# Performance work log

Measured on AMD Instinct MI355X. Metric: run time of the kernel, lower is better.

The kernel has to match this reference:

```python
import jax, jax.numpy as jnp
import numpy as np

STAGE_NUM = 5
BETA = 1.0
EPS = 1e-6


def _em_refine(cls, proto):
    # cls: [b, d]; proto: [k, d]. Matches torch einsum('bd,bkd->bk') with
    # batch-replicated prototypes == cls @ proto.T (no (b,k,d) materialization).
    p = proto
    for _ in range(STAGE_NUM):
        r = jax.nn.softmax(cls @ p.T, axis=1)          # [b, k]
        p = r.T @ cls                                   # [k, d]
        p = p / (jnp.linalg.norm(p, axis=1, keepdims=True) + EPS)
    return p


def setup_inputs() -> dict:
    key = jax.random.key(0)
    k1, k2 = jax.random.split(key)
    b, d, k = 8192, 1024, 512
    cls = jax.random.normal(k1, (b, d), dtype=jnp.float32)
    proto = jax.random.normal(k2, (k, d), dtype=jnp.float32)
    # __init__ normalizes prototypes to unit norm (with 1e-6 in denominator)
    proto = proto / (1e-6 + jnp.linalg.norm(proto, axis=1, keepdims=True))
    return {"cls": cls, "prototypes": proto}


def reference(cls, prototypes):
    # EM loop runs under torch.no_grad() -> stop_gradient here.
    new_proto = jax.lax.stop_gradient(_em_refine(cls, prototypes))  # [k, d]
    dot = cls @ new_proto.T                                          # [b, k]
    r = jax.nn.softmax(dot, axis=1)
    z_recon = r @ new_proto                                          # [b, d]
    z_out = BETA * z_recon + cls
    return (r, z_out)
```

## Files before the change

### kernel.cpp

```cpp
#include <hip/hip_runtime.h>

typedef short v8s __attribute__((ext_vector_type(8)));
typedef _Float16 v8h __attribute__((ext_vector_type(8)));
typedef float v4f __attribute__((ext_vector_type(4)));

typedef __attribute__((address_space(1))) const void* as1_void_cp;
typedef __attribute__((address_space(3))) void* as3_void_p;

__device__ __forceinline__ unsigned short f2bf(float x) {
  union { float f; unsigned int u; } v; v.f = x;
  unsigned int r = v.u + 0x7fffu + ((v.u >> 16) & 1u);
  return (unsigned short)(r >> 16);
}
__device__ __forceinline__ float bf2f(unsigned short h) {
  union { unsigned int u; float f; } v; v.u = ((unsigned int)h) << 16;
  return v.f;
}
__device__ __forceinline__ unsigned short f2h(float x) {
  _Float16 h = (_Float16)x;
  return __builtin_bit_cast(unsigned short, h);
}

template <bool ADD, bool F16>
__global__ __launch_bounds__(256) void gemm_bt(
    const unsigned short* __restrict__ A, const unsigned short* __restrict__ B,
    float* __restrict__ C, const float* __restrict__ Cadd,
    int N, int lda, int ldb, int klen, size_t csplit) {
  __shared__ __align__(16) unsigned short As[128 * 64];
  __shared__ __align__(16) unsigned short Bs[128 * 64];
  const int tid = threadIdx.x;
  const int bn = blockIdx.x * 128, bm = blockIdx.y * 128;
  const int k0 = blockIdx.z * klen;
  float* Cp = C + (size_t)blockIdx.z * csplit;

  const unsigned short* ag0 = A + (size_t)(bm + (tid >> 2)) * lda + ((tid & 3) << 3) + k0;
  const unsigned short* ag1 = ag0 + (size_t)64 * lda;
  const unsigned short* bg0 = B + (size_t)(bn + (tid >> 2)) * ldb + ((tid & 3) << 3) + k0;
  const unsigned short* bg1 = bg0 + (size_t)64 * ldb;
  unsigned short* al0 = As + tid * 8;
  unsigned short* al1 = As + 2048 + tid * 8;
  unsigned short* al2 = As + 4096 + tid * 8;
  unsigned short* al3 = As + 6144 + tid * 8;
  unsigned short* bl0 = Bs + tid * 8;
  unsigned short* bl1 = Bs + 2048 + tid * 8;
  unsigned short* bl2 = Bs + 4096 + tid * 8;
  unsigned short* bl3 = Bs + 6144 + tid * 8;

  const int lane = tid & 63;
  const int q = lane >> 4, m15 = lane & 15;
  const int w = tid >> 6;
  const int wr = (w >> 1) * 64, wc = (w & 1) * 64;

  v4f acc[4][4];
#pragma unroll
  for (int i = 0; i < 4; ++i)
#pragma unroll
    for (int j = 0; j < 4; ++j) acc[i][j] = 0.f;

  for (int kk = 0; kk < klen; kk += 64) {
    __builtin_amdgcn_global_load_lds((as1_void_cp)(ag0 + kk), (as3_void_p)al0, 16, 0, 0);
    __builtin_amdgcn_global_load_lds((as1_void_cp)(ag1 + kk), (as3_void_p)al1, 16, 0, 0);
    __builtin_amdgcn_global_load_lds((as1_void_cp)(ag0 + kk + 32), (as3_void_p)al2, 16, 0, 0);
    __builtin_amdgcn_global_load_lds((as1_void_cp)(ag1 + kk + 32), (as3_void_p)al3, 16, 0, 0);
    __builtin_amdgcn_global_load_lds((as1_void_cp)(bg0 + kk), (as3_void_p)bl0, 16, 0, 0);
    __builtin_amdgcn_global_load_lds((as1_void_cp)(bg1 + kk), (as3_void_p)bl1, 16, 0, 0);
    __builtin_amdgcn_global_load_lds((as1_void_cp)(bg0 + kk + 32), (as3_void_p)bl2, 16, 0, 0);
    __builtin_amdgcn_global_load_lds((as1_void_cp)(bg1 + kk + 32), (as3_void_p)bl3, 16, 0, 0);
    __syncthreads();
#pragma unroll
    for (int h = 0; h < 2; ++h) {
      v8s af[4], bf[4];
#pragma unroll
      for (int i = 0; i < 4; ++i)
        af[i] = *(const v8s*)(As + h * 4096 + (wr + i * 16 + m15) * 32 + q * 8);
#pragma unroll
      for (int j = 0; j < 4; ++j)
        bf[j] = *(const v8s*)(Bs + h * 4096 + (wc + j * 16 + m15) * 32 + q * 8);
#pragma unroll
      for (int i = 0; i < 4; ++i)
#pragma unroll
        for (int j = 0; j < 4; ++j) {
          if constexpr (F16)
            acc[i][j] = __builtin_amdgcn_mfma_f32_16x16x32_f16(
                __builtin_bit_cast(v8h, af[i]), __builtin_bit_cast(v8h, bf[j]), acc[i][j], 0, 0, 0);
          else
            acc[i][j] = __builtin_amdgcn_mfma_f32_16x16x32_bf16(af[i], bf[j], acc[i][j], 0, 0, 0);
        }
    }
    __syncthreads();
  }

#pragma unroll
  for (int i = 0; i < 4; ++i) {
#pragma unroll
    for (int j = 0; j < 4; ++j) {
      const int col = bn + wc + j * 16 + m15;
#pragma unroll
      for (int rr = 0; rr < 4; ++rr) {
        const int row = bm + wr + i * 16 + q * 4 + rr;
        const size_t idx = (size_t)row * N + col;
        float v = acc[i][j][rr];
        if (ADD) v += Cadd[idx];
        Cp[idx] = v;
      }
    }
  }
}

__global__ __launch_bounds__(256) void gemm_bt3(
    const unsigned short* __restrict__ Ah, const unsigned short* __restrict__ Al,
    const unsigned short* __restrict__ Bh, const unsigned short* __restrict__ Bl,
    float* __restrict__ C, int N, int lda, int ldb, int klen, size_t csplit) {
  __shared__ __align__(16) unsigned short Ash[128 * 32];
  __shared__ __align__(16) unsigned short Asl[128 * 32];
  __shared__ __align__(16) unsigned short Bsh[128 * 32];
  __shared__ __align__(16) unsigned short Bsl[128 * 32];
  const int tid = threadIdx.x;
  const int bn = blockIdx.x * 128, bm = blockIdx.y * 128;
  const int k0 = blockIdx.z * klen;
  float* Cp = C + (size_t)blockIdx.z * csplit;

  const size_t aoff = (size_t)(bm + (tid >> 2)) * lda + ((tid & 3) << 3) + k0;
  const size_t boff = (size_t)(bn + (tid >> 2)) * ldb + ((tid & 3) << 3) + k0;
  const unsigned short* agh0 = Ah + aoff;
  const unsigned short* agh1 = agh0 + (size_t)64 * lda;
  const unsigned short* agl0 = Al + aoff;
  const unsigned short* agl1 = agl0 + (size_t)64 * lda;
  const unsigned short* bgh0 = Bh + boff;
  const unsigned short* bgh1 = bgh0 + (size_t)64 * ldb;
  const unsigned short* bgl0 = Bl + boff;
  const unsigned short* bgl1 = bgl0 + (size_t)64 * ldb;

  const int lane = tid & 63;
  const int q = lane >> 4, m15 = lane & 15;
  const int w = tid >> 6;
  const int wr = (w >> 1) * 64, wc = (w & 1) * 64;

  v4f acc[4][4];
#pragma unroll
  for (int i = 0; i < 4; ++i)
#pragma unroll
    for (int j = 0; j < 4; ++j) acc[i][j] = 0.f;

  for (int kk = 0; kk < klen; kk += 32) {
    __builtin_amdgcn_global_load_lds((as1_void_cp)(agh0 + kk), (as3_void_p)(Ash + tid * 8), 16, 0, 0);
    __builtin_amdgcn_global_load_lds((as1_void_cp)(agh1 + kk), (as3_void_p)(Ash + 2048 + tid * 8), 16, 0, 0);
    __builtin_amdgcn_global_load_lds((as1_void_cp)(agl0 + kk), (as3_void_p)(Asl + tid * 8), 16, 0, 0);
    __builtin_amdgcn_global_load_lds((as1_void_cp)(agl1 + kk), (as3_void_p)(Asl + 2048 + tid * 8), 16, 0, 0);
    __builtin_amdgcn_global_load_lds((as1_void_cp)(bgh0 + kk), (as3_void_p)(Bsh + tid * 8), 16, 0, 0);
    __builtin_amdgcn_global_load_lds((as1_void_cp)(bgh1 + kk), (as3_void_p)(Bsh + 2048 + tid * 8), 16, 0, 0);
    __builtin_amdgcn_global_load_lds((as1_void_cp)(bgl0 + kk), (as3_void_p)(Bsl + tid * 8), 16, 0, 0);
    __builtin_amdgcn_global_load_lds((as1_void_cp)(bgl1 + kk), (as3_void_p)(Bsl + 2048 + tid * 8), 16, 0, 0);
    __syncthreads();
    v8s afh[4], afl[4], bfh[4], bfl[4];
#pragma unroll
    for (int i = 0; i < 4; ++i) {
      const int ro = (wr + i * 16 + m15) * 32 + q * 8;
      afh[i] = *(const v8s*)(Ash + ro);
      afl[i] = *(const v8s*)(Asl + ro);
    }
#pragma unroll
    for (int j = 0; j < 4; ++j) {
      const int ro = (wc + j * 16 + m15) * 32 + q * 8;
      bfh[j] = *(const v8s*)(Bsh + ro);
      bfl[j] = *(const v8s*)(Bsl + ro);
    }
#pragma unroll
    for (int i = 0; i < 4; ++i)
#pragma unroll
      for (int j = 0; j < 4; ++j) {
        acc[i][j] = __builtin_amdgcn_mfma_f32_16x16x32_bf16(afh[i], bfh[j], acc[i][j], 0, 0, 0);
        acc[i][j] = __builtin_amdgcn_mfma_f32_16x16x32_bf16(afh[i], bfl[j], acc[i][j], 0, 0, 0);
        acc[i][j] = __builtin_amdgcn_mfma_f32_16x16x32_bf16(afl[i], bfh[j], acc[i][j], 0, 0, 0);
      }
    __syncthreads();
  }

#pragma unroll
  for (int i = 0; i < 4; ++i) {
#pragma unroll
    for (int j = 0; j < 4; ++j) {
      const int col = bn + wc + j * 16 + m15;
#pragma unroll
      for (int rr = 0; rr < 4; ++rr) {
        const int row = bm + wr + i * 16 + q * 4 + rr;
        Cp[(size_t)row * N + col] = acc[i][j][rr];
      }
    }
  }
}

__global__ __launch_bounds__(256) void cast_split_transpose_cls(
    const float* __restrict__ cls,
    unsigned short* __restrict__ ch, unsigned short* __restrict__ cl,
    unsigned short* __restrict__ cTh, unsigned short* __restrict__ cTl) {
  __shared__ unsigned short th[64][72];
  __shared__ unsigned short tl[64][72];
  const int d0 = blockIdx.x * 64, b0 = blockIdx.y * 64;
  const int t = threadIdx.x;
#pragma unroll
  for (int i = 0; i < 4; ++i) {
    int flat = t + i * 256;
    int bl_ = flat >> 4;
    int dl = (flat & 15) << 2;
    float4 v = *(const float4*)(cls + (size_t)(b0 + bl_) * 1024 + d0 + dl);
    ushort4 h, l;
    h.x = f2bf(v.x); l.x = f2bf(v.x - bf2f(h.x));
    h.y = f2bf(v.y); l.y = f2bf(v.y - bf2f(h.y));
    h.z = f2bf(v.z); l.z = f2bf(v.z - bf2f(h.z));
    h.w = f2bf(v.w); l.w = f2bf(v.w - bf2f(h.w));
    *(ushort4*)(ch + (size_t)(b0 + bl_) * 1024 + d0 + dl) = h;
    *(ushort4*)(cl + (size_t)(b0 + bl_) * 1024 + d0 + dl) = l;
    th[bl_][dl] = h.x; th[bl_][dl + 1] = h.y; th[bl_][dl + 2] = h.z; th[bl_][dl + 3] = h.w;
    tl[bl_][dl] = l.x; tl[bl_][dl + 1] = l.y; tl[bl_][dl + 2] = l.z; tl[bl_][dl + 3] = l.w;
  }
  __syncthreads();
#pragma unroll
  for (int i = 0; i < 4; ++i) {
    int flat = t + i * 256;
    int dl = flat >> 4;
    int bl_ = (flat & 15) << 2;
    ushort4 h = make_ushort4(th[bl_][dl], th[bl_ + 1][dl], th[bl_ + 2][dl], th[bl_ + 3][dl]);
    ushort4 l = make_ushort4(tl[bl_][dl], tl[bl_ + 1][dl], tl[bl_ + 2][dl], tl[bl_ + 3][dl]);
    *(ushort4*)(cTh + (size_t)(d0 + dl) * 8192 + b0 + bl_) = h;
    *(ushort4*)(cTl + (size_t)(d0 + dl) * 8192 + b0 + bl_) = l;
  }
}

__global__ __launch_bounds__(256) void split_f32(const float* __restrict__ in,
                                                 unsigned short* __restrict__ hi,
                                                 unsigned short* __restrict__ lo) {
  const size_t i = (size_t)(blockIdx.x * blockDim.x + threadIdx.x) * 4;
  float4 v = *(const float4*)(in + i);
  ushort4 h, l;
  h.x = f2bf(v.x); l.x = f2bf(v.x - bf2f(h.x));
  h.y = f2bf(v.y); l.y = f2bf(v.y - bf2f(h.y));
  h.z = f2bf(v.z); l.z = f2bf(v.z - bf2f(h.z));
  h.w = f2bf(v.w); l.w = f2bf(v.w - bf2f(h.w));
  *(ushort4*)(hi + i) = h;
  *(ushort4*)(lo + i) = l;
}

__global__ __launch_bounds__(256) void fuse_to_f16_dual(
    const unsigned short* __restrict__ h0, const unsigned short* __restrict__ l0,
    unsigned short* __restrict__ o0,
    const unsigned short* __restrict__ h1, const unsigned short* __restrict__ l1,
    unsigned short* __restrict__ o1) {
  const int half = blockIdx.x >> 12;
  const unsigned short* hi = half ? h1 : h0;
  const unsigned short* lo = half ? l1 : l0;
  unsigned short* out = half ? o1 : o0;
  const size_t i = ((size_t)(blockIdx.x & 4095) * 256 + threadIdx.x) * 8;
  ushort4 ha = *(const ushort4*)(hi + i);
  ushort4 hb = *(const ushort4*)(hi + i + 4);
  ushort4 la = *(const ushort4*)(lo + i);
  ushort4 lb = *(const ushort4*)(lo + i + 4);
  ushort4 oa, ob;
  oa.x = f2h(bf2f(ha.x) + bf2f(la.x)); oa.y = f2h(bf2f(ha.y) + bf2f(la.y));
  oa.z = f2h(bf2f(ha.z) + bf2f(la.z)); oa.w = f2h(bf2f(ha.w) + bf2f(la.w));
  ob.x = f2h(bf2f(hb.x) + bf2f(lb.x)); ob.y = f2h(bf2f(hb.y) + bf2f(lb.y));
  ob.z = f2h(bf2f(hb.z) + bf2f(lb.z)); ob.w = f2h(bf2f(hb.w) + bf2f(lb.w));
  *(ushort4*)(out + i) = oa;
  *(ushort4*)(out + i + 4) = ob;
}

__device__ __forceinline__ void online_merge(float& m, float& s, float m2, float s2) {
  float nm = fmaxf(m, m2);
  s = s * __expf(m - nm) + s2 * __expf(m2 - nm);
  m = nm;
}

__global__ __launch_bounds__(256) void colsoftmax_stats(
    const float* __restrict__ SP0, const float* __restrict__ SP1,
    float4* __restrict__ MS) {
  __shared__ float4 red[4][64];
  const int lane = threadIdx.x & 63, w = threadIdx.x >> 6;
  const int b = blockIdx.x * 128 + lane * 2;
  const int c0 = blockIdx.y * 64 + w * 16;
  const float2* x0 = (const float2*)(SP0 + (size_t)c0 * 8192 + b);
  const float2* x1 = (const float2*)(SP1 + (size_t)c0 * 8192 + b);
  float m0 = -3.4e38f, m1 = -3.4e38f, s0 = 0.f, s1 = 0.f;
#pragma unroll
  for (int i = 0; i < 16; ++i) {
    float2 a = x0[(size_t)i * 4096];
    float2 bb = x1[(size_t)i * 4096];
    float v0 = a.x + bb.x, v1 = a.y + bb.y;
    float nm0 = fmaxf(m0, v0);
    s0 = s0 * __expf(m0 - nm0) + __expf(v0 - nm0); m0 = nm0;
    float nm1 = fmaxf(m1, v1);
    s1 = s1 * __expf(m1 - nm1) + __expf(v1 - nm1); m1 = nm1;
  }
  red[w][lane] = make_float4(m0, s0, m1, s1);
  __syncthreads();
  if (w == 0) {
#pragma unroll
    for (int k = 1; k < 4; ++k) {
      float4 r = red[k][lane];
      online_merge(m0, s0, r.x, r.y);
      online_merge(m1, s1, r.z, r.w);
    }
    MS[(size_t)blockIdx.y * 4096 + (b >> 1)] = make_float4(m0, s0, m1, s1);
  }
}

template <bool F16>
__global__ __launch_bounds__(256) void colsoftmax_write(
    const float* __restrict__ SP0, const float* __restrict__ SP1,
    const float4* __restrict__ MS,
    unsigned short* __restrict__ rh, unsigned short* __restrict__ rl) {
  const int lane = threadIdx.x & 63, w = threadIdx.x >> 6;
  const int b = blockIdx.x * 128 + lane * 2;
  const int c0 = blockIdx.y * 64 + w * 16;
  float m0 = -3.4e38f, m1 = -3.4e38f, s0 = 0.f, s1 = 0.f;
#pragma unroll
  for (int k = 0; k < 8; ++k) {
    float4 r = MS[(size_t)k * 4096 + (b >> 1)];
    online_merge(m0, s0, r.x, r.y);
    online_merge(m1, s1, r.z, r.w);
  }
  const float inv0 = 1.f / s0, inv1 = 1.f / s1;
  const float2* x0 = (const float2*)(SP0 + (size_t)c0 * 8192 + b);
  const float2* x1 = (const float2*)(SP1 + (size_t)c0 * 8192 + b);
#pragma unroll
  for (int i = 0; i < 16; ++i) {
    float2 a = x0[(size_t)i * 4096];
    float2 bb = x1[(size_t)i * 4096];
    float r0 = __expf(a.x + bb.x - m0) * inv0;
    float r1 = __expf(a.y + bb.y - m1) * inv1;
    const size_t idx = (size_t)(c0 + i) * 8192 + b;
    if constexpr (F16) {
      *(ushort2*)(rh + idx) = make_ushort2(f2h(r0), f2h(r1));
    } else {
      unsigned short h0 = f2bf(r0), h1 = f2bf(r1);
      *(ushort2*)(rh + idx) = make_ushort2(h0, h1);
      *(ushort2*)(rl + idx) = make_ushort2(f2bf(r0 - bf2f(h0)), f2bf(r1 - bf2f(h1)));
    }
  }
}

__global__ __launch_bounds__(256) void softmax_rows(const float* __restrict__ SP0,
                                                    const float* __restrict__ SP1,
                                                    float* __restrict__ r_out,
                                                    unsigned short* __restrict__ r_g) {
  const int w = threadIdx.x >> 6, lane = threadIdx.x & 63;
  const int row = blockIdx.x * 4 + w;
  const size_t off = (size_t)row * 512 + lane * 8;
  float4 v0 = *(const float4*)(SP0 + off);
  float4 v1 = *(const float4*)(SP0 + off + 4);
  float4 u0 = *(const float4*)(SP1 + off);
  float4 u1 = *(const float4*)(SP1 + off + 4);
  v0.x += u0.x; v0.y += u0.y; v0.z += u0.z; v0.w += u0.w;
  v1.x += u1.x; v1.y += u1.y; v1.z += u1.z; v1.w += u1.w;
  float m = fmaxf(fmaxf(fmaxf(v0.x, v0.y), fmaxf(v0.z, v0.w)),
                  fmaxf(fmaxf(v1.x, v1.y), fmaxf(v1.z, v1.w)));
  for (int off2 = 32; off2; off2 >>= 1) m = fmaxf(m, __shfl_xor(m, off2));
  float e0 = __expf(v0.x - m), e1 = __expf(v0.y - m), e2 = __expf(v0.z - m), e3 = __expf(v0.w - m);
  float e4 = __expf(v1.x - m), e5 = __expf(v1.y - m), e6 = __expf(v1.z - m), e7 = __expf(v1.w - m);
  float s = e0 + e1 + e2 + e3 + e4 + e5 + e6 + e7;
  for (int off2 = 32; off2; off2 >>= 1) s += __shfl_xor(s, off2);
  const float inv = 1.f / s;
  e0 *= inv; e1 *= inv; e2 *= inv; e3 *= inv; e4 *= inv; e5 *= inv; e6 *= inv; e7 *= inv;
  float* rp = r_out + off;
  *(float4*)rp = make_float4(e0, e1, e2, e3);
  *(float4*)(rp + 4) = make_float4(e4, e5, e6, e7);
  unsigned short* bp = r_g + off;
  *(ushort4*)bp = make_ushort4(f2h(e0), f2h(e1), f2h(e2), f2h(e3));
  *(ushort4*)(bp + 4) = make_ushort4(f2h(e4), f2h(e5), f2h(e6), f2h(e7));
}

__global__ __launch_bounds__(256) void reduce_normalize(const float* __restrict__ Pp,
                                                        unsigned short* __restrict__ pg,
                                                        unsigned short* __restrict__ pTg) {
  __shared__ float red[4];
  const int c = blockIdx.x, t = threadIdx.x;
  float ax = 0.f, ay = 0.f, az = 0.f, aw = 0.f;
#pragma unroll
  for (int s = 0; s < 16; ++s) {
    const float4 v = *(const float4*)(Pp + ((size_t)s * 512 + c) * 1024 + t * 4);
    ax += v.x; ay += v.y; az += v.z; aw += v.w;
  }
  float ss = ax * ax + ay * ay + az * az + aw * aw;
  for (int off = 32; off; off >>= 1) ss += __shfl_xor(ss, off);
  const int w = t >> 6, lane = t & 63;
  if (!lane) red[w] = ss;
  __syncthreads();
  const float tot = red[0] + red[1] + red[2] + red[3];
  const float scale = 1.f / (sqrtf(tot) + 1e-6f);
  ax *= scale; ay *= scale; az *= scale; aw *= scale;
  *(ushort4*)(pg + (size_t)c * 1024 + t * 4) =
      make_ushort4(f2h(ax), f2h(ay), f2h(az), f2h(aw));
  pTg[(size_t)(t * 4 + 0) * 512 + c] = f2h(ax);
  pTg[(size_t)(t * 4 + 1) * 512 + c] = f2h(ay);
  pTg[(size_t)(t * 4 + 2) * 512 + c] = f2h(az);
  pTg[(size_t)(t * 4 + 3) * 512 + c] = f2h(aw);
}

extern "C" void kernel_launch(void* const* d_in, const int* in_sizes, int n_in,
                              void* d_out, int out_size, void* d_ws, size_t ws_size,
                              hipStream_t stream) {
  const float* cls = (const float*)d_in[0];
  const float* proto = (const float*)d_in[1];
  float* out_r = (float*)d_out;
  float* out_z = out_r + (size_t)8192 * 512;

  char* w = (char*)d_ws;
  unsigned short* cls_h = (unsigned short*)w; w += (size_t)8192 * 1024 * 2;
  unsigned short* cls_l = (unsigned short*)w; w += (size_t)8192 * 1024 * 2;
  unsigned short* clsT_h = (unsigned short*)w; w += (size_t)1024 * 8192 * 2;
  unsigned short* clsT_l = (unsigned short*)w; w += (size_t)1024 * 8192 * 2;
  unsigned short* p_h = (unsigned short*)w; w += (size_t)512 * 1024 * 2;
  unsigned short* p_l = (unsigned short*)w; w += (size_t)512 * 1024 * 2;
  unsigned short* p_g = (unsigned short*)w; w += (size_t)512 * 1024 * 2;
  unsigned short* pT_g = (unsigned short*)w; w += (size_t)1024 * 512 * 2;
  unsigned short* rT_h = (unsigned short*)w; w += (size_t)512 * 8192 * 2;
  unsigned short* rT_l = (unsigned short*)w; w += (size_t)512 * 8192 * 2;
  float4* MS = (float4*)w; w += (size_t)8 * 4096 * 16;
  float* SP = (float*)w;
  float* SP1 = SP + (size_t)512 * 8192;
  unsigned short* cls_g = cls_l;
  unsigned short* clsT_g = clsT_l;

  cast_split_transpose_cls<<<dim3(16, 128), 256, 0, stream>>>(cls, cls_h, cls_l, clsT_h, clsT_l);
  split_f32<<<512, 256, 0, stream>>>(proto, p_h, p_l);

  gemm_bt3<<<dim3(64, 4, 2), 256, 0, stream>>>(p_h, p_l, cls_h, cls_l, SP,
                                               8192, 1024, 1024, 512,
                                               (size_t)512 * 8192);
  colsoftmax_stats<<<dim3(64, 8), 256, 0, stream>>>(SP, SP1, MS);
  colsoftmax_write<false><<<dim3(64, 8), 256, 0, stream>>>(SP, SP1, MS, rT_h, rT_l);
  gemm_bt3<<<dim3(8, 4, 16), 256, 0, stream>>>(rT_h, rT_l, clsT_h, clsT_l, SP,
                                               1024, 8192, 8192, 512,
                                               (size_t)512 * 1024);
  fuse_to_f16_dual<<<8192, 256, 0, stream>>>(cls_h, cls_l, cls_g, clsT_h, clsT_l, clsT_g);
  reduce_normalize<<<512, 256, 0, stream>>>(SP, p_g, pT_g);

  for (int it = 0; it < 4; ++it) {
    gemm_bt<false, true><<<dim3(64, 4, 2), 256, 0, stream>>>(p_g, cls_g, SP, nullptr,
                                                             8192, 1024, 1024, 512,
                                                             (size_t)512 * 8192);
    colsoftmax_stats<<<dim3(64, 8), 256, 0, stream>>>(SP, SP1, MS);
    colsoftmax_write<true><<<dim3(64, 8), 256, 0, stream>>>(SP, SP1, MS, rT_h, nullptr);
    gemm_bt<false, true><<<dim3(8, 4, 16), 256, 0, stream>>>(rT_h, clsT_g, SP, nullptr,
                                                             1024, 8192, 8192, 512,
                                                             (size_t)512 * 1024);
    reduce_normalize<<<512, 256, 0, stream>>>(SP, p_g, pT_g);
  }

  gemm_bt<false, true><<<dim3(4, 64, 2), 256, 0, stream>>>(cls_g, p_g, SP, nullptr,
                                                           512, 1024, 1024, 512,
                                                           (size_t)8192 * 512);
  softmax_rows<<<2048, 256, 0, stream>>>(SP, SP + (size_t)8192 * 512, out_r, rT_h);
  gemm_bt<true, true><<<dim3(8, 64, 1), 256, 0, stream>>>(rT_h, pT_g, out_z, cls,
                                                          1024, 512, 512, 512, 0);
}
```

Measured before the change: 494.6 us.

## Compute EM logits row-major and fuse row softmax with LDS transpose

The EM-step logits GEMM now produces a [b,k] row-major score matrix (operands swapped), so the softmax over k becomes a row softmax done in one kernel with wave shuffles. The result is transposed through shared memory and written as rT, replacing the two-pass column-softmax stats/write kernels and the MS scratch buffer. This removes one launch and one full re-read of the split-K partial scores per iteration. It costs a 33KB-66KB LDS tile per block, and the logits GEMM runs with a different output shape and grid. reduce_normalize_hl is added but never called.

After: 487.0 us. Within noise of the previous version (-1.5%).

```diff
diff --git a/kernel.cpp b/kernel.cpp
--- a/kernel.cpp
+++ b/kernel.cpp
@@ -264,77 +264,64 @@
   *(ushort4*)(out + i + 4) = ob;
 }
 
-__device__ __forceinline__ void online_merge(float& m, float& s, float m2, float s2) {
-  float nm = fmaxf(m, m2);
-  s = s * __expf(m - nm) + s2 * __expf(m2 - nm);
-  m = nm;
-}
-
-__global__ __launch_bounds__(256) void colsoftmax_stats(
+template <bool HILO>
+__global__ __launch_bounds__(512) void rowsoftmax_T(
     const float* __restrict__ SP0, const float* __restrict__ SP1,
-    float4* __restrict__ MS) {
-  __shared__ float4 red[4][64];
-  const int lane = threadIdx.x & 63, w = threadIdx.x >> 6;
-  const int b = blockIdx.x * 128 + lane * 2;
-  const int c0 = blockIdx.y * 64 + w * 16;
-  const float2* x0 = (const float2*)(SP0 + (size_t)c0 * 8192 + b);
-  const float2* x1 = (const float2*)(SP1 + (size_t)c0 * 8192 + b);
-  float m0 = -3.4e38f, m1 = -3.4e38f, s0 = 0.f, s1 = 0.f;
-#pragma unroll
-  for (int i = 0; i < 16; ++i) {
-    float2 a = x0[(size_t)i * 4096];
-    float2 bb = x1[(size_t)i * 4096];
-    float v0 = a.x + bb.x, v1 = a.y + bb.y;
-    float nm0 = fmaxf(m0, v0);
-    s0 = s0 * __expf(m0 - nm0) + __expf(v0 - nm0); m0 = nm0;
-    float nm1 = fmaxf(m1, v1);
-    s1 = s1 * __expf(m1 - nm1) + __expf(v1 - nm1); m1 = nm1;
-  }
-  red[w][lane] = make_float4(m0, s0, m1, s1);
+    unsigned short* __restrict__ rTh, unsigned short* __restrict__ rTl) {
+  __shared__ __align__(16) unsigned short th[32 * 520];
+  __shared__ __align__(16) unsigned short tl[HILO ? 32 * 520 : 8];
+  const int t = threadIdx.x;
+  const int lane = t & 63, w = t >> 6;
+  const int b0 = blockIdx.x * 32;
+#pragma unroll
+  for (int k = 0; k < 4; ++k) {
+    const int bl = w * 4 + k;
+    const int row = b0 + bl;
+    const size_t off = (size_t)row * 512 + lane * 8;
+    float4 v0 = *(const float4*)(SP0 + off);
+    float4 v1 = *(const float4*)(SP0 + off + 4);
+    float4 u0 = *(const float4*)(SP1 + off);
+    float4 u1 = *(const float4*)(SP1 + off + 4);
+    float e[8];
+    e[0] = v0.x + u0.x; e[1] = v0.y + u0.y; e[2] = v0.z + u0.z; e[3] = v0.w + u0.w;
+    e[4] = v1.x + u1.x; e[5] = v1.y + u1.y; e[6] = v1.z + u1.z; e[7] = v1.w + u1.w;
+    float m = fmaxf(fmaxf(fmaxf(e[0], e[1]), fmaxf(e[2], e[3])),
+                    fmaxf(fmaxf(e[4], e[5]), fmaxf(e[6], e[7])));
+    for (int o = 32; o; o >>= 1) m = fmaxf(m, __shfl_xor(m, o));
+    float s = 0.f;
+#pragma unroll
+    for (int i = 0; i < 8; ++i) { e[i] = __expf(e[i] - m); s += e[i]; }
+    for (int o = 32; o; o >>= 1) s += __shfl_xor(s, o);
+    const float inv = 1.f / s;
+    unsigned short ph[8], pl[8];
+#pragma unroll
+    for (int i = 0; i < 8; ++i) {
+      const float r = e[i] * inv;
+      if constexpr (HILO) {
+        ph[i] = f2bf(r);
+        pl[i] = f2bf(r - bf2f(ph[i]));
+      } else {
+        ph[i] = f2h(r);
+      }
+    }
+    *(v8s*)&th[bl * 520 + lane * 8] = *(v8s*)ph;
+    if constexpr (HILO) *(v8s*)&tl[bl * 520 + lane * 8] = *(v8s*)pl;
+  }
   __syncthreads();
-  if (w == 0) {
-#pragma unroll
-    for (int k = 1; k < 4; ++k) {
-      float4 r = red[k][lane];
-      online_merge(m0, s0, r.x, r.y);
-      online_merge(m1, s1, r.z, r.w);
-    }
-    MS[(size_t)blockIdx.y * 4096 + (b >> 1)] = make_float4(m0, s0, m1, s1);
-  }
-}
-
-template <bool F16>
-__global__ __launch_bounds__(256) void colsoftmax_write(
-    const float* __restrict__ SP0, const float* __restrict__ SP1,
-    const float4* __restrict__ MS,
-    unsigned short* __restrict__ rh, unsigned short* __restrict__ rl) {
-  const int lane = threadIdx.x & 63, w = threadIdx.x >> 6;
-  const int b = blockIdx.x * 128 + lane * 2;
-  const int c0 = blockIdx.y * 64 + w * 16;
-  float m0 = -3.4e38f, m1 = -3.4e38f, s0 = 0.f, s1 = 0.f;
-#pragma unroll
-  for (int k = 0; k < 8; ++k) {
-    float4 r = MS[(size_t)k * 4096 + (b >> 1)];
-    online_merge(m0, s0, r.x, r.y);
-    online_merge(m1, s1, r.z, r.w);
-  }
-  const float inv0 = 1.f / s0, inv1 = 1.f / s1;
-  const float2* x0 = (const float2*)(SP0 + (size_t)c0 * 8192 + b);
-  const float2* x1 = (const float2*)(SP1 + (size_t)c0 * 8192 + b);
-#pragma unroll
-  for (int i = 0; i < 16; ++i) {
-    float2 a = x0[(size_t)i * 4096];
-    float2 bb = x1[(size_t)i * 4096];
-    float r0 = __expf(a.x + bb.x - m0) * inv0;
-    float r1 = __expf(a.y + bb.y - m1) * inv1;
-    const size_t idx = (size_t)(c0 + i) * 8192 + b;
-    if constexpr (F16) {
-      *(ushort2*)(rh + idx) = make_ushort2(f2h(r0), f2h(r1));
-    } else {
-      unsigned short h0 = f2bf(r0), h1 = f2bf(r1);
-      *(ushort2*)(rh + idx) = make_ushort2(h0, h1);
-      *(ushort2*)(rl + idx) = make_ushort2(f2bf(r0 - bf2f(h0)), f2bf(r1 - bf2f(h1)));
-    }
+  const int c = t;
+  unsigned short uh[32];
+#pragma unroll
+  for (int b = 0; b < 32; ++b) uh[b] = th[b * 520 + c];
+#pragma unroll
+  for (int q = 0; q < 4; ++q)
+    *(v8s*)(rTh + (size_t)c * 8192 + b0 + q * 8) = *(v8s*)&uh[q * 8];
+  if constexpr (HILO) {
+    unsigned short ul[32];
+#pragma unroll
+    for (int b = 0; b < 32; ++b) ul[b] = tl[b * 520 + c];
+#pragma unroll
+    for (int q = 0; q < 4; ++q)
+      *(v8s*)(rTl + (size_t)c * 8192 + b0 + q * 8) = *(v8s*)&ul[q * 8];
   }
 }
 
@@ -395,6 +382,34 @@
   pTg[(size_t)(t * 4 + 3) * 512 + c] = f2h(aw);
 }
 
+__global__ __launch_bounds__(256) void reduce_normalize_hl(const float* __restrict__ Pp,
+                                                           unsigned short* __restrict__ ph,
+                                                           unsigned short* __restrict__ pl) {
+  __shared__ float red[4];
+  const int c = blockIdx.x, t = threadIdx.x;
+  float ax = 0.f, ay = 0.f, az = 0.f, aw = 0.f;
+#pragma unroll
+  for (int s = 0; s < 16; ++s) {
+    const float4 v = *(const float4*)(Pp + ((size_t)s * 512 + c) * 1024 + t * 4);
+    ax += v.x; ay += v.y; az += v.z; aw += v.w;
+  }
+  float ss = ax * ax + ay * ay + az * az + aw * aw;
+  for (int off = 32; off; off >>= 1) ss += __shfl_xor(ss, off);
+  const int w = t >> 6, lane = t & 63;
+  if (!lane) red[w] = ss;
+  __syncthreads();
+  const float tot = red[0] + red[1] + red[2] + red[3];
+  const float scale = 1.f / (sqrtf(tot) + 1e-6f);
+  ax *= scale; ay *= scale; az *= scale; aw *= scale;
+  ushort4 h, l;
+  h.x = f2bf(ax); l.x = f2bf(ax - bf2f(h.x));
+  h.y = f2bf(ay); l.y = f2bf(ay - bf2f(h.y));
+  h.z = f2bf(az); l.z = f2bf(az - bf2f(h.z));
+  h.w = f2bf(aw); l.w = f2bf(aw - bf2f(h.w));
+  *(ushort4*)(ph + (size_t)c * 1024 + t * 4) = h;
+  *(ushort4*)(pl + (size_t)c * 1024 + t * 4) = l;
+}
+
 extern "C" void kernel_launch(void* const* d_in, const int* in_sizes, int n_in,
                               void* d_out, int out_size, void* d_ws, size_t ws_size,
                               hipStream_t stream) {
@@ -414,20 +429,18 @@
   unsigned short* pT_g = (unsigned short*)w; w += (size_t)1024 * 512 * 2;
   unsigned short* rT_h = (unsigned short*)w; w += (size_t)512 * 8192 * 2;
   unsigned short* rT_l = (unsigned short*)w; w += (size_t)512 * 8192 * 2;
-  float4* MS = (float4*)w; w += (size_t)8 * 4096 * 16;
   float* SP = (float*)w;
-  float* SP1 = SP + (size_t)512 * 8192;
+  float* SP1 = SP + (size_t)8192 * 512;
   unsigned short* cls_g = cls_l;
   unsigned short* clsT_g = clsT_l;
 
   cast_split_transpose_cls<<<dim3(16, 128), 256, 0, stream>>>(cls, cls_h, cls_l, clsT_h, clsT_l);
   split_f32<<<512, 256, 0, stream>>>(proto, p_h, p_l);
 
-  gemm_bt3<<<dim3(64, 4, 2), 256, 0, stream>>>(p_h, p_l, cls_h, cls_l, SP,
-                                               8192, 1024, 1024, 512,
-                                               (size_t)512 * 8192);
-  colsoftmax_stats<<<dim3(64, 8), 256, 0, stream>>>(SP, SP1, MS);
-  colsoftmax_write<false><<<dim3(64, 8), 256, 0, stream>>>(SP, SP1, MS, rT_h, rT_l);
+  gemm_bt3<<<dim3(4, 64, 2), 256, 0, stream>>>(cls_h, cls_l, p_h, p_l, SP,
+                                               512, 1024, 1024, 512,
+                                               (size_t)8192 * 512);
+  rowsoftmax_T<true><<<256, 512, 0, stream>>>(SP, SP1, rT_h, rT_l);
   gemm_bt3<<<dim3(8, 4, 16), 256, 0, stream>>>(rT_h, rT_l, clsT_h, clsT_l, SP,
                                                1024, 8192, 8192, 512,
                                                (size_t)512 * 1024);
@@ -435,11 +448,10 @@
   reduce_normalize<<<512, 256, 0, stream>>>(SP, p_g, pT_g);
 
   for (int it = 0; it < 4; ++it) {
-    gemm_bt<false, true><<<dim3(64, 4, 2), 256, 0, stream>>>(p_g, cls_g, SP, nullptr,
-                                                             8192, 1024, 1024, 512,
-                                                             (size_t)512 * 8192);
-    colsoftmax_stats<<<dim3(64, 8), 256, 0, stream>>>(SP, SP1, MS);
-    colsoftmax_write<true><<<dim3(64, 8), 256, 0, stream>>>(SP, SP1, MS, rT_h, nullptr);
+    gemm_bt<false, true><<<dim3(4, 64, 2), 256, 0, stream>>>(cls_g, p_g, SP, nullptr,
+                                                             512, 1024, 1024, 512,
+                                                             (size_t)8192 * 512);
+    rowsoftmax_T<false><<<256, 512, 0, stream>>>(SP, SP1, rT_h, nullptr);
     gemm_bt<false, true><<<dim3(8, 4, 16), 256, 0, stream>>>(rT_h, clsT_g, SP, nullptr,
                                                              1024, 8192, 8192, 512,
                                                              (size_t)512 * 1024);
@@ -449,7 +461,7 @@
   gemm_bt<false, true><<<dim3(4, 64, 2), 256, 0, stream>>>(cls_g, p_g, SP, nullptr,
                                                            512, 1024, 1024, 512,
                                                            (size_t)8192 * 512);
-  softmax_rows<<<2048, 256, 0, stream>>>(SP, SP + (size_t)8192 * 512, out_r, rT_h);
+  softmax_rows<<<2048, 256, 0, stream>>>(SP, SP1, out_r, rT_h);
   gemm_bt<true, true><<<dim3(8, 64, 1), 256, 0, stream>>>(rT_h, pT_g, out_z, cls,
                                                           1024, 512, 512, 512, 0);
 }
```
